# Optimization experiments

Hardware: AMD Instinct MI355X
Metric: run time of the kernel (lower is better)

Reference implementation:

```python
import jax, jax.numpy as jnp
import numpy as np

N_NODES = 100000

def setup_inputs() -> dict:
    key = jax.random.key(0)
    k1, k2, k3, k4 = jax.random.split(key, 4)
    features = jax.random.normal(k1, (N_NODES, 128), dtype=jnp.float32)
    # Xavier-uniform init like the torch module
    limit = float(np.sqrt(6.0 / (128 + 64)))
    weight = jax.random.uniform(k2, (128, 64), dtype=jnp.float32, minval=-limit, maxval=limit)
    edge_index = jax.random.randint(k3, (2, 1600000), 0, N_NODES, dtype=jnp.int64)
    edge_weight = jax.random.uniform(k4, (1600000,), dtype=jnp.float32)
    return {"features": features, "weight": weight, "edge_index": edge_index, "edge_weight": edge_weight}

def reference(features, weight, edge_index, edge_weight):
    # support = X @ W  -> [N, out]
    support = features @ weight
    dst, src = edge_index[0], edge_index[1]
    # spmm(adj, support): out[i] = sum_j adj[i, j] * support[j]
    msgs = support[src] * edge_weight[:, None]            # [E, out]
    out = jax.ops.segment_sum(msgs, dst, num_segments=N_NODES)
    return jax.nn.relu(out)
```

## Files before the change

### kernel.cpp

```cpp
#include <hip/hip_runtime.h>
#include <hip/hip_bf16.h>

#define F_IN 128
#define F_OUT 64
#define NPB 128
#define LG_NPB 7
#define MAXB 1024
#define BIN_BLOCKS 400
#define BIN_THREADS 512
#define SORT_CAP 4096

#define GEMM_RT 256
#define GEMM_KC 16
#define XT_STRIDE (GEMM_RT + 4)

__global__ void __launch_bounds__(256) gnn_gemm_kernel(
    const float* __restrict__ X, const float* __restrict__ W,
    __hip_bfloat16* __restrict__ support, int n_rows) {
    __shared__ float Wlds[F_IN * F_OUT];
    __shared__ float Xt[GEMM_KC * XT_STRIDE];
    const int t = threadIdx.x;
    for (int i = t; i < F_IN * F_OUT; i += 256) Wlds[i] = W[i];

    const int row0 = blockIdx.x * GEMM_RT;
    const int ti = t >> 3;
    const int tj = t & 7;
    const int r0 = ti * 8;
    const int c0 = tj * 8;

    float acc[8][8];
#pragma unroll
    for (int r = 0; r < 8; ++r)
#pragma unroll
        for (int c = 0; c < 8; ++c) acc[r][c] = 0.f;

    for (int kc = 0; kc < F_IN; kc += GEMM_KC) {
        __syncthreads();
#pragma unroll
        for (int v = 0; v < 4; ++v) {
            const int idx = t + v * 256;
            const int r   = idx >> 2;
            const int k4  = (idx & 3) * 4;
            float4 xv = make_float4(0.f, 0.f, 0.f, 0.f);
            if (row0 + r < n_rows)
                xv = *reinterpret_cast<const float4*>(
                    X + (size_t)(row0 + r) * F_IN + kc + k4);
            Xt[(k4 + 0) * XT_STRIDE + r] = xv.x;
            Xt[(k4 + 1) * XT_STRIDE + r] = xv.y;
            Xt[(k4 + 2) * XT_STRIDE + r] = xv.z;
            Xt[(k4 + 3) * XT_STRIDE + r] = xv.w;
        }
        __syncthreads();
#pragma unroll 4
        for (int kk = 0; kk < GEMM_KC; ++kk) {
            const float4 xa = *reinterpret_cast<const float4*>(&Xt[kk * XT_STRIDE + r0]);
            const float4 xb = *reinterpret_cast<const float4*>(&Xt[kk * XT_STRIDE + r0 + 4]);
            const float4 wa = *reinterpret_cast<const float4*>(&Wlds[(kc + kk) * F_OUT + c0]);
            const float4 wb = *reinterpret_cast<const float4*>(&Wlds[(kc + kk) * F_OUT + c0 + 4]);
            const float xr[8] = {xa.x, xa.y, xa.z, xa.w, xb.x, xb.y, xb.z, xb.w};
            const float wc[8] = {wa.x, wa.y, wa.z, wa.w, wb.x, wb.y, wb.z, wb.w};
#pragma unroll
            for (int r = 0; r < 8; ++r)
#pragma unroll
                for (int c = 0; c < 8; ++c)
                    acc[r][c] = fmaf(xr[r], wc[c], acc[r][c]);
        }
    }

#pragma unroll
    for (int r = 0; r < 8; ++r) {
        const int row = row0 + r0 + r;
        if (row < n_rows) {
            union { __hip_bfloat16 h[8]; uint4 u; } pk;
#pragma unroll
            for (int c = 0; c < 8; ++c) pk.h[c] = __float2bfloat16(acc[r][c]);
            *reinterpret_cast<uint4*>(support + (size_t)row * F_OUT + c0) = pk.u;
        }
    }
}

__global__ void __launch_bounds__(BIN_THREADS) gnn_bhist_kernel(
    const int* __restrict__ dst, int* __restrict__ gcounts, int n_edges, int n_buckets) {
    __shared__ int lcnt[MAXB];
    const int t = threadIdx.x;
    for (int i = t; i < MAXB; i += BIN_THREADS) lcnt[i] = 0;
    __syncthreads();
    const int chunk = (n_edges + gridDim.x - 1) / gridDim.x;
    const int c0 = blockIdx.x * chunk;
    const int c1 = min(c0 + chunk, n_edges);
    for (int i = c0 + t; i < c1; i += BIN_THREADS)
        atomicAdd(&lcnt[dst[i] >> LG_NPB], 1);
    __syncthreads();
    for (int b = t; b < n_buckets; b += BIN_THREADS)
        if (lcnt[b]) atomicAdd(&gcounts[b], lcnt[b]);
}

__global__ void __launch_bounds__(1024) gnn_bscan_kernel(
    const int* __restrict__ gcounts, int* __restrict__ starts,
    int* __restrict__ cursor, int n_buckets) {
    __shared__ int s[1024];
    const int t = threadIdx.x;
    const int v = (t < n_buckets) ? gcounts[t] : 0;
    s[t] = v;
    __syncthreads();
    for (int off = 1; off < 1024; off <<= 1) {
        int x = (t >= off) ? s[t - off] : 0;
        __syncthreads();
        s[t] += x;
        __syncthreads();
    }
    if (t < n_buckets) {
        const int st = s[t] - v;
        starts[t] = st;
        cursor[t] = st;
    }
}

__global__ void __launch_bounds__(BIN_THREADS) gnn_place_kernel(
    const int* __restrict__ ei, const float* __restrict__ ew,
    int* __restrict__ cursor, int2* __restrict__ elistA, int n_edges, int n_buckets) {
    __shared__ int lcnt[MAXB];
    const int t = threadIdx.x;
    for (int i = t; i < MAXB; i += BIN_THREADS) lcnt[i] = 0;
    __syncthreads();
    const int chunk = (n_edges + gridDim.x - 1) / gridDim.x;
    const int c0 = blockIdx.x * chunk;
    const int c1 = min(c0 + chunk, n_edges);
    for (int i = c0 + t; i < c1; i += BIN_THREADS)
        atomicAdd(&lcnt[ei[i] >> LG_NPB], 1);
    __syncthreads();
    for (int b = t; b < n_buckets; b += BIN_THREADS) {
        const int c = lcnt[b];
        if (c) lcnt[b] = atomicAdd(&cursor[b], c);
    }
    __syncthreads();
    for (int i = c0 + t; i < c1; i += BIN_THREADS) {
        const int d = ei[i];
        const int s = ei[n_edges + i];
        const float w = ew[i];
        const int b = d >> LG_NPB;
        const int pos = atomicAdd(&lcnt[b], 1);
        elistA[pos] = make_int2((s << LG_NPB) | (d & (NPB - 1)), __float_as_int(w));
    }
}

__global__ void __launch_bounds__(512) gnn_sortpull_kernel(
    const __hip_bfloat16* __restrict__ support, const int2* __restrict__ elistA,
    const int* __restrict__ starts, const int* __restrict__ gcounts,
    float* __restrict__ out, int n_nodes) {
    __shared__ int2 smeta[SORT_CAP];
    __shared__ int hist[NPB];
    __shared__ int pfx[NPB];
    __shared__ int segs[NPB + 1];
    __shared__ int cur[NPB];
    const int t = threadIdx.x;
    const int b = blockIdx.x;
    const int bstart = starts[b];
    const int cnt    = min(gcounts[b], SORT_CAP);

    if (t < NPB) hist[t] = 0;
    __syncthreads();
    for (int i = t; i < cnt; i += 512)
        atomicAdd(&hist[elistA[bstart + i].x & (NPB - 1)], 1);
    __syncthreads();

    if (t < NPB) pfx[t] = hist[t];
    __syncthreads();
    for (int off = 1; off < NPB; off <<= 1) {
        int x = 0;
        if (t < NPB && t >= off) x = pfx[t - off];
        __syncthreads();
        if (t < NPB) pfx[t] += x;
        __syncthreads();
    }
    if (t < NPB) {
        const int st = pfx[t] - hist[t];
        segs[t] = st;
        cur[t]  = st;
    }
    if (t == 0) segs[NPB] = cnt;
    __syncthreads();

    for (int i = t; i < cnt; i += 512) {
        const int2 m = elistA[bstart + i];
        const int dlo = m.x & (NPB - 1);
        const int pos = atomicAdd(&cur[dlo], 1);
        smeta[pos] = make_int2(m.x >> LG_NPB, m.y);
    }
    __syncthreads();

    const int lane = t & 63;
    const int wave = t >> 6;
    for (int n = wave; n < NPB; n += 8) {
        const int node = b * NPB + n;
        if (node >= n_nodes) break;
        int e  = segs[n];
        const int e1 = segs[n + 1];
        float acc = 0.f;
        for (; e + 8 <= e1; e += 8) {
            int2 m[8];
#pragma unroll
            for (int u = 0; u < 8; ++u) m[u] = smeta[e + u];
            float g[8];
#pragma unroll
            for (int u = 0; u < 8; ++u)
                g[u] = __bfloat162float(support[(size_t)m[u].x * F_OUT + lane]);
#pragma unroll
            for (int u = 0; u < 8; ++u)
                acc = fmaf(__int_as_float(m[u].y), g[u], acc);
        }
        for (; e + 2 <= e1; e += 2) {
            const int2 m0 = smeta[e];
            const int2 m1 = smeta[e + 1];
            const float g0 = __bfloat162float(support[(size_t)m0.x * F_OUT + lane]);
            const float g1 = __bfloat162float(support[(size_t)m1.x * F_OUT + lane]);
            acc = fmaf(__int_as_float(m0.y), g0, acc);
            acc = fmaf(__int_as_float(m1.y), g1, acc);
        }
        if (e < e1) {
            const int2 m0 = smeta[e];
            acc = fmaf(__int_as_float(m0.y),
                       __bfloat162float(support[(size_t)m0.x * F_OUT + lane]), acc);
        }
        out[(size_t)node * F_OUT + lane] = fmaxf(acc, 0.f);
    }
}

extern "C" void kernel_launch(void* const* d_in, const int* in_sizes, int n_in,
                              void* d_out, int out_size, void* d_ws, size_t ws_size,
                              hipStream_t stream) {
    const float* X  = (const float*)d_in[0];
    const float* W  = (const float*)d_in[1];
    const int*   EI = (const int*)d_in[2];
    const float* EW = (const float*)d_in[3];
    float*       out = (float*)d_out;

    const int n_edges   = in_sizes[2] / 2;
    const int n_rows    = in_sizes[0] / F_IN;
    const int n_nodes   = out_size / F_OUT;
    const int n_buckets = (n_nodes + NPB - 1) >> LG_NPB;

    char* ws = (char*)d_ws;
    __hip_bfloat16* support = (__hip_bfloat16*)ws;
    size_t off = (size_t)n_rows * F_OUT * sizeof(__hip_bfloat16);
    int2* elistA = (int2*)(ws + off); off += (size_t)n_edges * sizeof(int2);
    int* gcounts = (int*)(ws + off);  off += MAXB * sizeof(int);
    int* starts  = (int*)(ws + off);  off += MAXB * sizeof(int);
    int* cursor  = (int*)(ws + off);

    hipMemsetAsync(gcounts, 0, (size_t)n_buckets * sizeof(int), stream);

    gnn_bhist_kernel<<<BIN_BLOCKS, BIN_THREADS, 0, stream>>>(EI, gcounts, n_edges, n_buckets);
    gnn_bscan_kernel<<<1, 1024, 0, stream>>>(gcounts, starts, cursor, n_buckets);
    gnn_place_kernel<<<BIN_BLOCKS, BIN_THREADS, 0, stream>>>(EI, EW, cursor, elistA, n_edges, n_buckets);
    gnn_gemm_kernel<<<(n_rows + GEMM_RT - 1) / GEMM_RT, 256, 0, stream>>>(X, W, support, n_rows);
    gnn_sortpull_kernel<<<n_buckets, 512, 0, stream>>>(support, elistA, starts, gcounts, out, n_nodes);
}
```

Baseline: 215.4 us.

## Halve GEMM row tile, vectorize edge binning loads, precompute byte offsets

```diff
diff --git a/kernel.cpp b/kernel.cpp
--- a/kernel.cpp
+++ b/kernel.cpp
@@ -10,7 +10,7 @@
 #define BIN_THREADS 512
 #define SORT_CAP 4096
 
-#define GEMM_RT 256
+#define GEMM_RT 128
 #define GEMM_KC 16
 #define XT_STRIDE (GEMM_RT + 4)
 
@@ -25,19 +25,19 @@
     const int row0 = blockIdx.x * GEMM_RT;
     const int ti = t >> 3;
     const int tj = t & 7;
-    const int r0 = ti * 8;
+    const int r0 = ti * 4;
     const int c0 = tj * 8;
 
-    float acc[8][8];
-#pragma unroll
-    for (int r = 0; r < 8; ++r)
+    float acc[4][8];
+#pragma unroll
+    for (int r = 0; r < 4; ++r)
 #pragma unroll
         for (int c = 0; c < 8; ++c) acc[r][c] = 0.f;
 
     for (int kc = 0; kc < F_IN; kc += GEMM_KC) {
         __syncthreads();
 #pragma unroll
-        for (int v = 0; v < 4; ++v) {
+        for (int v = 0; v < 2; ++v) {
             const int idx = t + v * 256;
             const int r   = idx >> 2;
             const int k4  = (idx & 3) * 4;
@@ -54,13 +54,12 @@
 #pragma unroll 4
         for (int kk = 0; kk < GEMM_KC; ++kk) {
             const float4 xa = *reinterpret_cast<const float4*>(&Xt[kk * XT_STRIDE + r0]);
-            const float4 xb = *reinterpret_cast<const float4*>(&Xt[kk * XT_STRIDE + r0 + 4]);
             const float4 wa = *reinterpret_cast<const float4*>(&Wlds[(kc + kk) * F_OUT + c0]);
             const float4 wb = *reinterpret_cast<const float4*>(&Wlds[(kc + kk) * F_OUT + c0 + 4]);
-            const float xr[8] = {xa.x, xa.y, xa.z, xa.w, xb.x, xb.y, xb.z, xb.w};
+            const float xr[4] = {xa.x, xa.y, xa.z, xa.w};
             const float wc[8] = {wa.x, wa.y, wa.z, wa.w, wb.x, wb.y, wb.z, wb.w};
 #pragma unroll
-            for (int r = 0; r < 8; ++r)
+            for (int r = 0; r < 4; ++r)
 #pragma unroll
                 for (int c = 0; c < 8; ++c)
                     acc[r][c] = fmaf(xr[r], wc[c], acc[r][c]);
@@ -68,7 +67,7 @@
     }
 
 #pragma unroll
-    for (int r = 0; r < 8; ++r) {
+    for (int r = 0; r < 4; ++r) {
         const int row = row0 + r0 + r;
         if (row < n_rows) {
             union { __hip_bfloat16 h[8]; uint4 u; } pk;
@@ -85,10 +84,20 @@
     const int t = threadIdx.x;
     for (int i = t; i < MAXB; i += BIN_THREADS) lcnt[i] = 0;
     __syncthreads();
-    const int chunk = (n_edges + gridDim.x - 1) / gridDim.x;
-    const int c0 = blockIdx.x * chunk;
+    int chunk = (n_edges + gridDim.x - 1) / gridDim.x;
+    chunk = (chunk + 3) & ~3;
+    const int c0 = min((int)(blockIdx.x * chunk), n_edges);
     const int c1 = min(c0 + chunk, n_edges);
-    for (int i = c0 + t; i < c1; i += BIN_THREADS)
+    const int nv = (c1 - c0) >> 2;
+    const int4* d4 = reinterpret_cast<const int4*>(dst + c0);
+    for (int i = t; i < nv; i += BIN_THREADS) {
+        const int4 d = d4[i];
+        atomicAdd(&lcnt[d.x >> LG_NPB], 1);
+        atomicAdd(&lcnt[d.y >> LG_NPB], 1);
+        atomicAdd(&lcnt[d.z >> LG_NPB], 1);
+        atomicAdd(&lcnt[d.w >> LG_NPB], 1);
+    }
+    for (int i = c0 + (nv << 2) + t; i < c1; i += BIN_THREADS)
         atomicAdd(&lcnt[dst[i] >> LG_NPB], 1);
     __syncthreads();
     for (int b = t; b < n_buckets; b += BIN_THREADS)
@@ -123,10 +132,21 @@
     const int t = threadIdx.x;
     for (int i = t; i < MAXB; i += BIN_THREADS) lcnt[i] = 0;
     __syncthreads();
-    const int chunk = (n_edges + gridDim.x - 1) / gridDim.x;
-    const int c0 = blockIdx.x * chunk;
+    int chunk = (n_edges + gridDim.x - 1) / gridDim.x;
+    chunk = (chunk + 3) & ~3;
+    const int c0 = min((int)(blockIdx.x * chunk), n_edges);
     const int c1 = min(c0 + chunk, n_edges);
-    for (int i = c0 + t; i < c1; i += BIN_THREADS)
+    const int nv = (c1 - c0) >> 2;
+    const int4* d4 = reinterpret_cast<const int4*>(ei + c0);
+
+    for (int i = t; i < nv; i += BIN_THREADS) {
+        const int4 d = d4[i];
+        atomicAdd(&lcnt[d.x >> LG_NPB], 1);
+        atomicAdd(&lcnt[d.y >> LG_NPB], 1);
+        atomicAdd(&lcnt[d.z >> LG_NPB], 1);
+        atomicAdd(&lcnt[d.w >> LG_NPB], 1);
+    }
+    for (int i = c0 + (nv << 2) + t; i < c1; i += BIN_THREADS)
         atomicAdd(&lcnt[ei[i] >> LG_NPB], 1);
     __syncthreads();
     for (int b = t; b < n_buckets; b += BIN_THREADS) {
@@ -134,13 +154,31 @@
         if (c) lcnt[b] = atomicAdd(&cursor[b], c);
     }
     __syncthreads();
-    for (int i = c0 + t; i < c1; i += BIN_THREADS) {
+
+    const int4*   s4 = reinterpret_cast<const int4*>(ei + n_edges + c0);
+    const float4* w4 = reinterpret_cast<const float4*>(ew + c0);
+    for (int i = t; i < nv; i += BIN_THREADS) {
+        const int4 d = d4[i];
+        const int4 s = s4[i];
+        const float4 w = w4[i];
+        const int dd[4] = {d.x, d.y, d.z, d.w};
+        const int ss[4] = {s.x, s.y, s.z, s.w};
+        const float ww[4] = {w.x, w.y, w.z, w.w};
+#pragma unroll
+        for (int u = 0; u < 4; ++u) {
+            const int b = dd[u] >> LG_NPB;
+            const int pos = atomicAdd(&lcnt[b], 1);
+            elistA[pos] = make_int2((ss[u] << LG_NPB) | (dd[u] & (NPB - 1)),
+                                    __float_as_int(ww[u]));
+        }
+    }
+    for (int i = c0 + (nv << 2) + t; i < c1; i += BIN_THREADS) {
         const int d = ei[i];
         const int s = ei[n_edges + i];
-        const float w = ew[i];
         const int b = d >> LG_NPB;
         const int pos = atomicAdd(&lcnt[b], 1);
-        elistA[pos] = make_int2((s << LG_NPB) | (d & (NPB - 1)), __float_as_int(w));
+        elistA[pos] = make_int2((s << LG_NPB) | (d & (NPB - 1)),
+                                __float_as_int(ew[i]));
     }
 }
 
@@ -185,10 +223,11 @@
         const int2 m = elistA[bstart + i];
         const int dlo = m.x & (NPB - 1);
         const int pos = atomicAdd(&cur[dlo], 1);
-        smeta[pos] = make_int2(m.x >> LG_NPB, m.y);
-    }
-    __syncthreads();
-
+        smeta[pos] = make_int2(m.x & ~(NPB - 1), m.y);
+    }
+    __syncthreads();
+
+    const char* sp = reinterpret_cast<const char*>(support);
     const int lane = t & 63;
     const int wave = t >> 6;
     for (int n = wave; n < NPB; n += 8) {
@@ -204,7 +243,8 @@
             float g[8];
 #pragma unroll
             for (int u = 0; u < 8; ++u)
-                g[u] = __bfloat162float(support[(size_t)m[u].x * F_OUT + lane]);
+                g[u] = __bfloat162float(
+                    *reinterpret_cast<const __hip_bfloat16*>(sp + m[u].x + lane * 2));
 #pragma unroll
             for (int u = 0; u < 8; ++u)
                 acc = fmaf(__int_as_float(m[u].y), g[u], acc);
@@ -212,15 +252,19 @@
         for (; e + 2 <= e1; e += 2) {
             const int2 m0 = smeta[e];
             const int2 m1 = smeta[e + 1];
-            const float g0 = __bfloat162float(support[(size_t)m0.x * F_OUT + lane]);
-            const float g1 = __bfloat162float(support[(size_t)m1.x * F_OUT + lane]);
+            const float g0 = __bfloat162float(
+                *reinterpret_cast<const __hip_bfloat16*>(sp + m0.x + lane * 2));
+            const float g1 = __bfloat162float(
+                *reinterpret_cast<const __hip_bfloat16*>(sp + m1.x + lane * 2));
             acc = fmaf(__int_as_float(m0.y), g0, acc);
             acc = fmaf(__int_as_float(m1.y), g1, acc);
         }
         if (e < e1) {
             const int2 m0 = smeta[e];
             acc = fmaf(__int_as_float(m0.y),
-                       __bfloat162float(support[(size_t)m0.x * F_OUT + lane]), acc);
+                       __bfloat162float(
+                           *reinterpret_cast<const __hip_bfloat16*>(sp + m0.x + lane * 2)),
+                       acc);
         }
         out[(size_t)node * F_OUT + lane] = fmaxf(acc, 0.f);
     }
```

After: 202.8 us. 1.06x faster.
